# Optimization experiments

Hardware: AMD Instinct MI355X
Metric: run time of the kernel (lower is better)

Reference implementation:

```python
import jax, jax.numpy as jnp
import numpy as np

DEPTH, DIM, HEADS, MLP_HID, POS_DIM, PROJ_DIM, NCLS, INP = 5, 128, 8, 256, 128, 128, 1000, 35
EPS = 1e-5

def _ln(x, g, b):
    m = x.mean(-1, keepdims=True)
    v = ((x - m) ** 2).mean(-1, keepdims=True)
    return (x - m) / jnp.sqrt(v + EPS) * g + b

def _gelu(x):
    return jax.nn.gelu(x, approximate=False)  # torch nn.GELU default (erf)

def setup_inputs() -> dict:
    key = jax.random.key(0)
    ks = iter(jax.random.split(key, 80))
    nxt = lambda: next(ks)
    B, N = 8, 1024
    w = lambda *s: (jax.random.normal(nxt(), s, jnp.float32) / np.sqrt(s[-2]).astype(np.float32))
    z = lambda *s: jnp.zeros(s, jnp.float32)
    o = lambda *s: jnp.ones(s, jnp.float32)
    node_feat = jax.random.normal(nxt(), (B, N, 3), jnp.float32)
    a = (jax.random.uniform(nxt(), (B, N, N)) < 0.01).astype(jnp.float32)
    adj = jnp.maximum(a, a.transpose(0, 2, 1))  # symmetric 0/1 adjacency
    lapl = jax.random.normal(nxt(), (B, N, 32), jnp.float32) * 0.1
    d = dict(
        node_feat=node_feat, adj=adj, lapl=lapl,
        cls_token=jax.random.normal(nxt(), (1, 1, DIM), jnp.float32),
        pe_w1=w(INP, 2 * INP), pe_b1=z(2 * INP),
        pe_w2=w(2 * INP, 2 * INP), pe_b2=z(2 * INP),
        pe_w3=w(2 * INP, 2 * INP), pe_b3=z(2 * INP),
        pe_lng=o(2 * INP), pe_lnb=z(2 * INP),
        pe_w4=w(2 * INP, POS_DIM), pe_b4=z(POS_DIM),
        blk_ln1_g=o(DEPTH, DIM), blk_ln1_b=z(DEPTH, DIM),
        blk_qkv_w=w(DEPTH, DIM, 3 * HEADS * DIM),
        blk_proj_w=w(DEPTH, HEADS * DIM, DIM), blk_proj_b=z(DEPTH, DIM),
        blk_gamma_w=jax.random.uniform(nxt(), (DEPTH, DIM, 2), jnp.float32) * 0.01,
        blk_gamma_b=z(DEPTH, 2),
        blk_ln2_g=o(DEPTH, DIM), blk_ln2_b=z(DEPTH, DIM),
        blk_mlp_w1=w(DEPTH, DIM, MLP_HID), blk_mlp_b1=z(DEPTH, MLP_HID),
        blk_mlp_w2=w(DEPTH, MLP_HID, DIM), blk_mlp_b2=z(DEPTH, DIM),
        head_lng=o(DIM), head_lnb=z(DIM), head_w=w(DIM, DIM), head_b=z(DIM),
        proj_w1=w(DIM, PROJ_DIM), proj_b1=z(PROJ_DIM),
        proj_w2=w(PROJ_DIM, PROJ_DIM), proj_b2=z(PROJ_DIM),
        proj_w3=w(PROJ_DIM, PROJ_DIM), proj_b3=z(PROJ_DIM),
        proj_lng=o(PROJ_DIM), proj_lnb=z(PROJ_DIM),
        proj_w4=w(PROJ_DIM, NCLS), proj_b4=z(NCLS),
    )
    return d

def reference(node_feat, adj, lapl, cls_token, pe_w1, pe_b1, pe_w2, pe_b2, pe_w3, pe_b3,
              pe_lng, pe_lnb, pe_w4, pe_b4, blk_ln1_g, blk_ln1_b, blk_qkv_w, blk_proj_w,
              blk_proj_b, blk_gamma_w, blk_gamma_b, blk_ln2_g, blk_ln2_b, blk_mlp_w1,
              blk_mlp_b1, blk_mlp_w2, blk_mlp_b2, head_lng, head_lnb, head_w, head_b,
              proj_w1, proj_b1, proj_w2, proj_b2, proj_w3, proj_b3, proj_lng, proj_lnb,
              proj_w4, proj_b4):
    B, N, _ = node_feat.shape
    M = N + 1
    # positional-encoding MLP on concatenated [node_feat | lapl] (inp_dim = 35)
    x = jnp.concatenate([node_feat, lapl], axis=2)
    x = _gelu(x @ pe_w1 + pe_b1)
    x = _gelu(x @ pe_w2 + pe_b2)
    x = _gelu(x @ pe_w3 + pe_b3)
    x = _ln(x, pe_lng, pe_lnb) @ pe_w4 + pe_b4  # [B,N,DIM]
    x = jnp.concatenate([jnp.broadcast_to(cls_token, (B, 1, DIM)), x], axis=1)  # [B,M,DIM]
    # adjacency with cls row/col, adj_cls[:,0,0] = 1
    adj_cls = jnp.zeros((B, M, M), x.dtype).at[:, 0, 0].set(1.0).at[:, 1:, 1:].set(adj)
    scale = DIM ** (-0.5)
    for i in range(DEPTH):
        h = _ln(x, blk_ln1_g[i], blk_ln1_b[i])
        qkv = (h @ blk_qkv_w[i]).reshape(B, M, 3, HEADS, DIM).transpose(2, 0, 3, 1, 4)
        q, k, v = qkv[0], qkv[1], qkv[2]  # each [B,H,M,D]
        attn = jnp.einsum('bhnd,bhmd->bhnm', q, k) * scale
        gamma = jnp.exp(h @ blk_gamma_w[i] + blk_gamma_b[i])  # [B,M,2], use_exp=True
        attn = gamma[:, None, :, 0:1] * attn + gamma[:, None, :, 1:2] * adj_cls[:, None]
        attn = jax.nn.softmax(attn, axis=-1)
        o = jnp.einsum('bhnm,bhmd->bhnd', attn, v).transpose(0, 2, 1, 3).reshape(B, M, HEADS * DIM)
        x = o @ blk_proj_w[i] + blk_proj_b[i] + h  # residual from normed input (as in source)
        h2 = _ln(x, blk_ln2_g[i], blk_ln2_b[i])
        x = _gelu(h2 @ blk_mlp_w1[i] + blk_mlp_b1[i]) @ blk_mlp_w2[i] + blk_mlp_b2[i] + h2
    c = x[:, 0]
    c = _ln(c, head_lng, head_lnb) @ head_w + head_b  # mlp_head
    p = _gelu(c @ proj_w1 + proj_b1)
    p = _gelu(p @ proj_w2 + proj_b2)
    p = _gelu(p @ proj_w3 + proj_b3)
    p = _ln(p, proj_lng, proj_lnb) @ proj_w4 + proj_b4
    return (c, p)
```

## Files before the change

### kernel.cpp

```cpp
#include <hip/hip_runtime.h>
#include <hip/hip_bf16.h>
#include <math.h>

#define NB 8
#define NSEQ 1024
#define M_ 1025
#define ROWS (NB * M_)
#define DIMC 128
#define NHEADS 8
#define QKV3 3072
#define PEROWS (NB * NSEQ)
#define ACS 1088

typedef __attribute__((ext_vector_type(8))) short bf16x8;
typedef __attribute__((ext_vector_type(4))) float f32x4;

__device__ __forceinline__ float gelu_f(float x) {
  return 0.5f * x * (1.f + erff(x * 0.70710678118654752440f));
}

__device__ __forceinline__ unsigned short f2bf(float f) {
  __hip_bfloat16 h = __float2bfloat16(f);
  return *reinterpret_cast<unsigned short*>(&h);
}

__device__ __forceinline__ float bf2f(unsigned short u) {
  union { unsigned int i; float f; } c;
  c.i = ((unsigned int)u) << 16;
  return c.f;
}

template<int TR>
__global__ __launch_bounds__(256) void rowgemm_k(
    const float* __restrict__ in, const float* __restrict__ W,
    const float* __restrict__ bias, const float* __restrict__ res,
    float* __restrict__ out, int rows, int K, int Nout, int act, int remap)
{
  extern __shared__ float s_in[];
  const int tid = threadIdx.x;
  const int r0 = blockIdx.x * TR;
  const int tot = TR * K;
  for (int idx = tid; idx < tot; idx += blockDim.x) {
    int r = idx / K;
    int k = idx - r * K;
    int gr = r0 + r;
    s_in[idx] = (gr < rows) ? in[(size_t)gr * K + k] : 0.f;
  }
  __syncthreads();
  const int j = blockIdx.y * blockDim.x + tid;
  if (j >= Nout) return;
  float acc[TR];
  const float bv = bias ? bias[j] : 0.f;
#pragma unroll
  for (int r = 0; r < TR; ++r) acc[r] = bv;
  for (int k = 0; k < K; ++k) {
    const float w = W[(size_t)k * Nout + j];
#pragma unroll
    for (int r = 0; r < TR; ++r) acc[r] = fmaf(s_in[r * K + k], w, acc[r]);
  }
  for (int r = 0; r < TR; ++r) {
    const int gr = r0 + r;
    if (gr >= rows) break;
    float v = acc[r];
    if (act == 1) v = gelu_f(v);
    if (res) v += res[(size_t)gr * Nout + j];
    const size_t orow = remap ? (size_t)(gr + gr / 1024 + 1) : (size_t)gr;
    out[orow * (size_t)Nout + j] = v;
  }
}

template<int ACT, int OBF, int RES>
__global__ __launch_bounds__(256) void mgemm_k(
    const unsigned short* __restrict__ Xb, const unsigned short* __restrict__ Wt,
    const float* __restrict__ bias, const float* __restrict__ res,
    void* __restrict__ outp, int rows, int K, int N)
{
  __shared__ unsigned short sX[64][72];
  __shared__ unsigned short sW[64][72];
  const int tid = threadIdx.x;
  const int w = tid >> 6, lane = tid & 63;
  const int col = lane & 15, quad = lane >> 4;
  const int r0 = blockIdx.x * 64, n0 = blockIdx.y * 64;
  const int lr = tid >> 2, lc = tid & 3;
  const int xrow = min(r0 + lr, rows - 1);
  const unsigned short* xsrc = Xb + (size_t)xrow * K + lc * 8;
  const unsigned short* wsrc = Wt + (size_t)(n0 + lr) * K + lc * 8;

  f32x4 acc[4];
#pragma unroll
  for (int t = 0; t < 4; ++t) acc[t] = (f32x4){0.f, 0.f, 0.f, 0.f};

  for (int k0 = 0; k0 < K; k0 += 64) {
    __syncthreads();
    *(uint4*)&sX[lr][lc * 8]      = *(const uint4*)(xsrc + k0);
    *(uint4*)&sX[lr][lc * 8 + 32] = *(const uint4*)(xsrc + k0 + 32);
    *(uint4*)&sW[lr][lc * 8]      = *(const uint4*)(wsrc + k0);
    *(uint4*)&sW[lr][lc * 8 + 32] = *(const uint4*)(wsrc + k0 + 32);
    __syncthreads();
    const bf16x8 aX0 = *(const bf16x8*)&sX[w * 16 + col][quad * 8];
    const bf16x8 aX1 = *(const bf16x8*)&sX[w * 16 + col][32 + quad * 8];
#pragma unroll
    for (int t = 0; t < 4; ++t) {
      const bf16x8 bW0 = *(const bf16x8*)&sW[t * 16 + col][quad * 8];
      const bf16x8 bW1 = *(const bf16x8*)&sW[t * 16 + col][32 + quad * 8];
      acc[t] = __builtin_amdgcn_mfma_f32_16x16x32_bf16(aX0, bW0, acc[t], 0, 0, 0);
      acc[t] = __builtin_amdgcn_mfma_f32_16x16x32_bf16(aX1, bW1, acc[t], 0, 0, 0);
    }
  }
  const int gr_base = r0 + w * 16 + quad * 4;
#pragma unroll
  for (int t = 0; t < 4; ++t) {
    const int n = n0 + t * 16 + col;
    const float bv = bias ? bias[n] : 0.f;
#pragma unroll
    for (int r = 0; r < 4; ++r) {
      const int gr = gr_base + r;
      if (gr < rows) {
        float v = acc[t][r] + bv;
        if (ACT) v = gelu_f(v);
        if (RES) v += res[(size_t)gr * N + n];
        if (OBF) ((unsigned short*)outp)[(size_t)gr * N + n] = f2bf(v);
        else     ((float*)outp)[(size_t)gr * N + n] = v;
      }
    }
  }
}

template<int OBF>
__global__ __launch_bounds__(256) void mgemm128_k(
    const unsigned short* __restrict__ Xb, const unsigned short* __restrict__ Wt,
    const float* __restrict__ bias, void* __restrict__ outp,
    int rows, int K, int N)
{
  __shared__ unsigned short sX[128][72];
  __shared__ unsigned short sW[128][72];
  const int tid = threadIdx.x;
  const int w = tid >> 6, lane = tid & 63;
  const int col = lane & 15, quad = lane >> 4;
  const int wr = w >> 1, wc = w & 1;
  const int r0 = blockIdx.x * 128, n0 = blockIdx.y * 128;

  f32x4 acc[4][4];
#pragma unroll
  for (int i = 0; i < 4; ++i)
#pragma unroll
    for (int j = 0; j < 4; ++j) acc[i][j] = (f32x4){0.f, 0.f, 0.f, 0.f};

  for (int k0 = 0; k0 < K; k0 += 64) {
    __syncthreads();
#pragma unroll
    for (int l = 0; l < 4; ++l) {
      const int idx = l * 256 + tid;
      const int row = idx >> 3, c = idx & 7;
      const int xrow = min(r0 + row, rows - 1);
      *(uint4*)&sX[row][c * 8] = *(const uint4*)(Xb + (size_t)xrow * K + k0 + c * 8);
      *(uint4*)&sW[row][c * 8] = *(const uint4*)(Wt + (size_t)(n0 + row) * K + k0 + c * 8);
    }
    __syncthreads();
    bf16x8 aX[4][2];
#pragma unroll
    for (int i = 0; i < 4; ++i) {
      aX[i][0] = *(const bf16x8*)&sX[wr * 64 + i * 16 + col][quad * 8];
      aX[i][1] = *(const bf16x8*)&sX[wr * 64 + i * 16 + col][32 + quad * 8];
    }
#pragma unroll
    for (int j = 0; j < 4; ++j) {
      const bf16x8 b0 = *(const bf16x8*)&sW[wc * 64 + j * 16 + col][quad * 8];
      const bf16x8 b1 = *(const bf16x8*)&sW[wc * 64 + j * 16 + col][32 + quad * 8];
#pragma unroll
      for (int i = 0; i < 4; ++i) {
        acc[i][j] = __builtin_amdgcn_mfma_f32_16x16x32_bf16(aX[i][0], b0, acc[i][j], 0, 0, 0);
        acc[i][j] = __builtin_amdgcn_mfma_f32_16x16x32_bf16(aX[i][1], b1, acc[i][j], 0, 0, 0);
      }
    }
  }
#pragma unroll
  for (int i = 0; i < 4; ++i) {
    const int gr_base = r0 + wr * 64 + i * 16 + quad * 4;
#pragma unroll
    for (int j = 0; j < 4; ++j) {
      const int n = n0 + wc * 64 + j * 16 + col;
      const float bv = bias ? bias[n] : 0.f;
#pragma unroll
      for (int r = 0; r < 4; ++r) {
        const int gr = gr_base + r;
        if (gr < rows) {
          const float v = acc[i][j][r] + bv;
          if (OBF) ((unsigned short*)outp)[(size_t)gr * N + n] = f2bf(v);
          else     ((float*)outp)[(size_t)gr * N + n] = v;
        }
      }
    }
  }
}

__global__ __launch_bounds__(256) void ln_rows_k(
    const float* __restrict__ in, float* __restrict__ out,
    unsigned short* __restrict__ outb,
    const float* __restrict__ g, const float* __restrict__ b,
    const float* __restrict__ gw, const float* __restrict__ gb,
    float* __restrict__ gamout, int rows, int D)
{
  const int wv = (blockIdx.x * blockDim.x + threadIdx.x) >> 6;
  const int lane = threadIdx.x & 63;
  if (wv >= rows) return;
  const float* r = in + (size_t)wv * D;
  float s = 0.f;
  for (int d = lane; d < D; d += 64) s += r[d];
  for (int off = 32; off; off >>= 1) s += __shfl_down(s, off);
  const float mean = __shfl(s, 0) / (float)D;
  float v = 0.f;
  for (int d = lane; d < D; d += 64) { float t = r[d] - mean; v += t * t; }
  for (int off = 32; off; off >>= 1) v += __shfl_down(v, off);
  const float inv = rsqrtf(__shfl(v, 0) / (float)D + 1e-5f);
  float* orow = out + (size_t)wv * D;
  float a0 = 0.f, a1 = 0.f;
  for (int d = lane; d < D; d += 64) {
    const float o = (r[d] - mean) * inv * g[d] + b[d];
    orow[d] = o;
    if (outb) outb[(size_t)wv * D + d] = f2bf(o);
    if (gw) { a0 = fmaf(o, gw[2 * d], a0); a1 = fmaf(o, gw[2 * d + 1], a1); }
  }
  if (gw) {
    for (int off = 32; off; off >>= 1) { a0 += __shfl_down(a0, off); a1 += __shfl_down(a1, off); }
    if (lane == 0) {
      gamout[(size_t)wv * 2 + 0] = expf(a0 + gb[0]);
      gamout[(size_t)wv * 2 + 1] = expf(a1 + gb[1]);
    }
  }
}

__global__ void adjc_k(const float* __restrict__ adj, unsigned short* __restrict__ adjc)
{
  const int n = blockIdx.x;
  const int b = blockIdx.y;
  unsigned short* row = adjc + ((size_t)b * M_ + n) * ACS;
  const float* ar = (n >= 1) ? adj + ((size_t)b * NSEQ + (n - 1)) * NSEQ : nullptr;
  for (int m = threadIdx.x; m < ACS; m += 256) {
    float v = 0.f;
    if (n == 0) v = (m == 0) ? 1.f : 0.f;
    else if (m >= 1 && m <= NSEQ) v = ar[m - 1];
    row[m] = f2bf(v);
  }
}

__global__ void wtrans_k(const float* __restrict__ W, unsigned short* __restrict__ Wt,
                         int K, int N)
{
  __shared__ float t[32][33];
  const int k0 = blockIdx.x * 32, n0 = blockIdx.y * 32;
  const float* Wd = W + (size_t)blockIdx.z * K * N;
  unsigned short* Wtd = Wt + (size_t)blockIdx.z * K * N;
  for (int i = threadIdx.y; i < 32; i += 8)
    t[i][threadIdx.x] = Wd[(size_t)(k0 + i) * N + n0 + threadIdx.x];
  __syncthreads();
  for (int i = threadIdx.y; i < 32; i += 8)
    Wtd[(size_t)(n0 + i) * K + k0 + threadIdx.x] = f2bf(t[threadIdx.x][i]);
}

__global__ __launch_bounds__(256) void vtrans_k(
    const unsigned short* __restrict__ qkv, unsigned short* __restrict__ vt)
{
  __shared__ unsigned short sT[64][136];
  const int mt = blockIdx.x, hh = blockIdx.y, b = blockIdx.z;
  const int tid = threadIdx.x;
  const int m0 = mt * 64;
#pragma unroll
  for (int l = 0; l < 4; ++l) {
    const int idx = l * 256 + tid;
    const int m = idx >> 4, c = idx & 15;
    const int gm = m0 + m;
    uint4 v = make_uint4(0u, 0u, 0u, 0u);
    if (gm < M_) v = *(const uint4*)(qkv + ((size_t)(b * M_ + gm)) * QKV3 + 2048 + hh * DIMC + c * 8);
    *(uint4*)&sT[m][c * 8] = v;
  }
  __syncthreads();
#pragma unroll
  for (int l = 0; l < 4; ++l) {
    const int idx = l * 256 + tid;
    const int d = idx >> 3, mc = idx & 7;
    unsigned short tmp[8];
#pragma unroll
    for (int j = 0; j < 8; ++j) tmp[j] = sT[mc * 8 + j][d];
    *(uint4*)(vt + (((size_t)(b * NHEADS + hh) * DIMC + d) * ACS) + m0 + mc * 8) = *(uint4*)tmp;
  }
}

__global__ __launch_bounds__(256) void attn_mfma_k(
    const unsigned short* __restrict__ qkv, const float* __restrict__ gamma,
    const unsigned short* __restrict__ adjc, const unsigned short* __restrict__ vt,
    unsigned short* __restrict__ o)
{
  __shared__ unsigned short sK[64][136];
  __shared__ unsigned short sVt[128][72];
  __shared__ unsigned short sP[64][72];

  const int hh = blockIdx.x, qt = blockIdx.y, b = blockIdx.z;
  const int tid = threadIdx.x;
  const int w = tid >> 6;
  const int lane = tid & 63;
  const int col = lane & 15;
  const int quad = lane >> 4;
  const int n0 = qt * 64;
  const int qbase = n0 + w * 16;
  const float scale = 0.088388347648318447f;

  bf16x8 aQ[4];
  {
    const int qrow = min(qbase + col, 1024);
    const unsigned short* qp = qkv + ((size_t)(b * M_ + qrow)) * QKV3 + hh * DIMC + quad * 8;
#pragma unroll
    for (int c = 0; c < 4; ++c) aQ[c] = *(const bf16x8*)(qp + c * 32);
  }
  float g0[4], g1[4];
  const unsigned short* adjr[4];
#pragma unroll
  for (int r = 0; r < 4; ++r) {
    const int nc = min(qbase + quad * 4 + r, 1024);
    g0[r] = gamma[(size_t)(b * M_ + nc) * 2 + 0] * scale;
    g1[r] = gamma[(size_t)(b * M_ + nc) * 2 + 1];
    adjr[r] = adjc + ((size_t)b * M_ + nc) * ACS;
  }

  float l_i[4] = {0.f, 0.f, 0.f, 0.f};
  f32x4 Oacc[8];
#pragma unroll
  for (int t = 0; t < 8; ++t) Oacc[t] = (f32x4){0.f, 0.f, 0.f, 0.f};

  const size_t vtbase = ((size_t)(b * NHEADS + hh)) * DIMC * ACS;

  for (int kt = 0; kt < 17; ++kt) {
    const int m0 = kt * 64;
    __syncthreads();
#pragma unroll
    for (int l = 0; l < 4; ++l) {
      const int idx = l * 256 + tid;
      {
        const int m = idx >> 4, c = idx & 15;
        const int gm = m0 + m;
        uint4 kv = make_uint4(0u, 0u, 0u, 0u);
        if (gm < M_) kv = *(const uint4*)(qkv + ((size_t)(b * M_ + gm)) * QKV3 + 1024 + hh * DIMC + c * 8);
        *(uint4*)&sK[m][c * 8] = kv;
      }
      {
        const int d = idx >> 3, mc = idx & 7;
        const uint4 vv = *(const uint4*)(vt + vtbase + (size_t)d * ACS + m0 + mc * 8);
        const int swc = mc ^ ((d >> 3) & 7);
        *(uint4*)&sVt[d][swc * 8] = vv;
      }
    }
    __syncthreads();

    f32x4 Sacc[4];
#pragma unroll
    for (int t = 0; t < 4; ++t) Sacc[t] = (f32x4){0.f, 0.f, 0.f, 0.f};
#pragma unroll
    for (int t = 0; t < 4; ++t) {
#pragma unroll
      for (int c = 0; c < 4; ++c) {
        const bf16x8 bK = *(const bf16x8*)&sK[t * 16 + col][c * 32 + quad * 8];
        Sacc[t] = __builtin_amdgcn_mfma_f32_16x16x32_bf16(aQ[c], bK, Sacc[t], 0, 0, 0);
      }
    }

#pragma unroll
    for (int t = 0; t < 4; ++t) {
      const int m = m0 + t * 16 + col;
      const bool mv = (m < M_);
      const int chb = t * 2 + (col >> 3);
#pragma unroll
      for (int r = 0; r < 4; ++r) {
        const float av = bf2f(adjr[r][m]);
        const float s = fmaf(g0[r], Sacc[t][r], g1[r] * av);
        const float pv = mv ? __expf(s) : 0.f;
        l_i[r] += pv;
        const int ql = w * 16 + quad * 4 + r;
        sP[ql][((chb ^ (ql & 7)) * 8) + (col & 7)] = f2bf(pv);
      }
    }

#pragma unroll
    for (int ch = 0; ch < 2; ++ch) {
      const int r0a = w * 16 + col;
      const bf16x8 aP = *(const bf16x8*)&sP[r0a][(((ch * 4 + quad) ^ (col & 7)) * 8)];
#pragma unroll
      for (int t = 0; t < 8; ++t) {
        const int pc = (ch * 4 + quad) ^ ((t * 2 + (col >> 3)) & 7);
        const bf16x8 bV = *(const bf16x8*)&sVt[t * 16 + col][pc * 8];
        Oacc[t] = __builtin_amdgcn_mfma_f32_16x16x32_bf16(aP, bV, Oacc[t], 0, 0, 0);
      }
    }
  }

#pragma unroll
  for (int r = 0; r < 4; ++r) {
    float s = l_i[r];
    s += __shfl_xor(s, 1);
    s += __shfl_xor(s, 2);
    s += __shfl_xor(s, 4);
    s += __shfl_xor(s, 8);
    const int n = qbase + quad * 4 + r;
    if (n < M_) {
      const float invl = 1.f / s;
      unsigned short* orow = o + ((size_t)(b * M_ + n)) * (NHEADS * DIMC) + hh * DIMC + col;
#pragma unroll
      for (int t = 0; t < 8; ++t) orow[t * 16] = f2bf(Oacc[t][r] * invl);
    }
  }
}

__global__ void concat_pe_k(const float* __restrict__ nf, const float* __restrict__ lp,
                            float* __restrict__ x35, int rows)
{
  const int idx = blockIdx.x * blockDim.x + threadIdx.x;
  if (idx >= rows * 35) return;
  const int r = idx / 35, c = idx - r * 35;
  x35[idx] = (c < 3) ? nf[(size_t)r * 3 + c] : lp[(size_t)r * 32 + (c - 3)];
}

__global__ void fill_cls_k(const float* __restrict__ cls, float* __restrict__ x)
{
  x[(size_t)blockIdx.x * M_ * DIMC + threadIdx.x] = cls[threadIdx.x];
}

__global__ void extract_cls_k(const float* __restrict__ x, float* __restrict__ c0)
{
  c0[(size_t)blockIdx.x * DIMC + threadIdx.x] = x[(size_t)blockIdx.x * M_ * DIMC + threadIdx.x];
}

extern "C" void kernel_launch(void* const* d_in, const int* in_sizes, int n_in,
                              void* d_out, int out_size, void* d_ws, size_t ws_size,
                              hipStream_t stream)
{
  (void)in_sizes; (void)n_in; (void)out_size; (void)ws_size;
  const float* node_feat = (const float*)d_in[0];
  const float* adj       = (const float*)d_in[1];
  const float* lapl      = (const float*)d_in[2];
  const float* cls_token = (const float*)d_in[3];
  const float* pe_w1 = (const float*)d_in[4];
  const float* pe_b1 = (const float*)d_in[5];
  const float* pe_w2 = (const float*)d_in[6];
  const float* pe_b2 = (const float*)d_in[7];
  const float* pe_w3 = (const float*)d_in[8];
  const float* pe_b3 = (const float*)d_in[9];
  const float* pe_lng = (const float*)d_in[10];
  const float* pe_lnb = (const float*)d_in[11];
  const float* pe_w4 = (const float*)d_in[12];
  const float* pe_b4 = (const float*)d_in[13];
  const float* blk_ln1_g = (const float*)d_in[14];
  const float* blk_ln1_b = (const float*)d_in[15];
  const float* blk_qkv_w = (const float*)d_in[16];
  const float* blk_proj_w = (const float*)d_in[17];
  const float* blk_proj_b = (const float*)d_in[18];
  const float* blk_gamma_w = (const float*)d_in[19];
  const float* blk_gamma_b = (const float*)d_in[20];
  const float* blk_ln2_g = (const float*)d_in[21];
  const float* blk_ln2_b = (const float*)d_in[22];
  const float* blk_mlp_w1 = (const float*)d_in[23];
  const float* blk_mlp_b1 = (const float*)d_in[24];
  const float* blk_mlp_w2 = (const float*)d_in[25];
  const float* blk_mlp_b2 = (const float*)d_in[26];
  const float* head_lng = (const float*)d_in[27];
  const float* head_lnb = (const float*)d_in[28];
  const float* head_w = (const float*)d_in[29];
  const float* head_b = (const float*)d_in[30];
  const float* proj_w1 = (const float*)d_in[31];
  const float* proj_b1 = (const float*)d_in[32];
  const float* proj_w2 = (const float*)d_in[33];
  const float* proj_b2 = (const float*)d_in[34];
  const float* proj_w3 = (const float*)d_in[35];
  const float* proj_b3 = (const float*)d_in[36];
  const float* proj_lng = (const float*)d_in[37];
  const float* proj_lnb = (const float*)d_in[38];
  const float* proj_w4 = (const float*)d_in[39];
  const float* proj_b4 = (const float*)d_in[40];

  float* ws   = (float*)d_ws;
  float* x    = ws;
  float* h    = x + 1049600;
  float* gam  = h + 1049600;
  float* obuf = gam + 16400;
  unsigned short* obufb = (unsigned short*)obuf;
  unsigned short* hidb  = (unsigned short*)(obuf + 4198400);
  float* x35 = obuf;
  float* xa  = obuf + 300000;
  float* xb  = obuf + 900000;
  float* sm  = obuf + 5248000;
  unsigned short* hb   = (unsigned short*)(sm + 8192);
  unsigned short* qkv  = hb + 1049600;
  unsigned short* adjc = qkv + 25190400;
  unsigned short* vt   = adjc + 8921600;
  unsigned short* qkvWt = vt + 8912896;
  unsigned short* projWt = qkvWt + 5 * 393216;
  unsigned short* mlp1Wt = projWt + 5 * 131072;
  unsigned short* mlp2Wt = mlp1Wt + 5 * 32768;
  float* s0 = sm, *s1 = sm + 1024, *s2 = sm + 2048, *s3 = sm + 3072;

  float* out_c = (float*)d_out;
  float* out_p = out_c + NB * DIMC;

  adjc_k<<<dim3(M_, NB), 256, 0, stream>>>(adj, adjc);
  wtrans_k<<<dim3(4, 96, 5), dim3(32, 8), 0, stream>>>(blk_qkv_w, qkvWt, 128, 3072);
  wtrans_k<<<dim3(32, 4, 5), dim3(32, 8), 0, stream>>>(blk_proj_w, projWt, 1024, 128);
  wtrans_k<<<dim3(4, 8, 5), dim3(32, 8), 0, stream>>>(blk_mlp_w1, mlp1Wt, 128, 256);
  wtrans_k<<<dim3(8, 4, 5), dim3(32, 8), 0, stream>>>(blk_mlp_w2, mlp2Wt, 256, 128);

  concat_pe_k<<<(PEROWS * 35 + 255) / 256, 256, 0, stream>>>(node_feat, lapl, x35, PEROWS);
  rowgemm_k<16><<<dim3(512, 1), 128, 16 * 35 * 4, stream>>>(x35, pe_w1, pe_b1, nullptr, xa, PEROWS, 35, 70, 1, 0);
  rowgemm_k<16><<<dim3(512, 1), 128, 16 * 70 * 4, stream>>>(xa, pe_w2, pe_b2, nullptr, xb, PEROWS, 70, 70, 1, 0);
  rowgemm_k<16><<<dim3(512, 1), 128, 16 * 70 * 4, stream>>>(xb, pe_w3, pe_b3, nullptr, xa, PEROWS, 70, 70, 1, 0);
  ln_rows_k<<<(PEROWS * 64 + 255) / 256, 256, 0, stream>>>(xa, xb, nullptr, pe_lng, pe_lnb, nullptr, nullptr, nullptr, PEROWS, 70);
  rowgemm_k<16><<<dim3(512, 1), 128, 16 * 70 * 4, stream>>>(xb, pe_w4, pe_b4, nullptr, x, PEROWS, 70, DIMC, 0, 1);
  fill_cls_k<<<NB, DIMC, 0, stream>>>(cls_token, x);

  const int lnGrid = (ROWS * 64 + 255) / 256;
  for (int i = 0; i < 5; ++i) {
    const float* ln1g = blk_ln1_g + i * DIMC;
    const float* ln1b = blk_ln1_b + i * DIMC;
    const float* pb   = blk_proj_b + i * DIMC;
    const float* gw   = blk_gamma_w + (size_t)i * DIMC * 2;
    const float* gb   = blk_gamma_b + i * 2;
    const float* ln2g = blk_ln2_g + i * DIMC;
    const float* ln2b = blk_ln2_b + i * DIMC;
    const float* mb1  = blk_mlp_b1 + i * 256;
    const float* mb2  = blk_mlp_b2 + i * DIMC;
    const unsigned short* qw = qkvWt + (size_t)i * 393216;
    const unsigned short* pw = projWt + (size_t)i * 131072;
    const unsigned short* m1w = mlp1Wt + (size_t)i * 32768;
    const unsigned short* m2w = mlp2Wt + (size_t)i * 32768;

    ln_rows_k<<<lnGrid, 256, 0, stream>>>(x, h, hb, ln1g, ln1b, gw, gb, gam, ROWS, DIMC);
    mgemm128_k<1><<<dim3(65, 24), 256, 0, stream>>>(hb, qw, nullptr, qkv, ROWS, 128, 3072);
    vtrans_k<<<dim3(17, NHEADS, NB), 256, 0, stream>>>(qkv, vt);
    attn_mfma_k<<<dim3(NHEADS, 17, NB), 256, 0, stream>>>(qkv, gam, adjc, vt, obufb);
    mgemm_k<0, 0, 1><<<dim3(129, 2), 256, 0, stream>>>(obufb, pw, pb, h, x, ROWS, 1024, 128);
    ln_rows_k<<<lnGrid, 256, 0, stream>>>(x, h, hb, ln2g, ln2b, nullptr, nullptr, nullptr, ROWS, DIMC);
    mgemm_k<1, 1, 0><<<dim3(129, 4), 256, 0, stream>>>(hb, m1w, mb1, nullptr, hidb, ROWS, 128, 256);
    mgemm_k<0, 0, 1><<<dim3(129, 2), 256, 0, stream>>>(hidb, m2w, mb2, h, x, ROWS, 256, 128);
  }

  extract_cls_k<<<NB, DIMC, 0, stream>>>(x, s0);
  ln_rows_k<<<2, 256, 0, stream>>>(s0, s1, nullptr, head_lng, head_lnb, nullptr, nullptr, nullptr, NB, DIMC);
  rowgemm_k<8><<<dim3(1, 1), 128, 8 * 128 * 4, stream>>>(s1, head_w, head_b, nullptr, out_c, NB, DIMC, DIMC, 0, 0);
  rowgemm_k<8><<<dim3(1, 1), 128, 8 * 128 * 4, stream>>>(out_c, proj_w1, proj_b1, nullptr, s2, NB, DIMC, DIMC, 1, 0);
  rowgemm_k<8><<<dim3(1, 1), 128, 8 * 128 * 4, stream>>>(s2, proj_w2, proj_b2, nullptr, s3, NB, DIMC, DIMC, 1, 0);
  rowgemm_k<8><<<dim3(1, 1), 128, 8 * 128 * 4, stream>>>(s3, proj_w3, proj_b3, nullptr, s2, NB, DIMC, DIMC, 1, 0);
  ln_rows_k<<<2, 256, 0, stream>>>(s2, s3, nullptr, proj_lng, proj_lnb, nullptr, nullptr, nullptr, NB, DIMC);
  rowgemm_k<8><<<dim3(1, 4), 256, 8 * 128 * 4, stream>>>(s3, proj_w4, proj_b4, nullptr, out_p, NB, DIMC, 1000, 0, 0);
}
```

Measured before the change: 1.622 ms.

## Bit-pack adjacency mask and run attention as a two-tile-per-block grid

Replaces the dense bf16 adjacency matrix with a 64-bit ballot bitmask per row and 64-column chunk. The attention kernel loads one mask word per row per key tile instead of gathering bf16 values from global memory, which cuts adjacency traffic roughly sixteenfold. The attention grid is also flattened to 544 blocks, each processing two (head, query-tile, batch) tiles in sequence. This reduces block count and may affect load balance and occupancy.

New measurement: 1.821 ms. 1.12x slower.

```diff
diff --git a/kernel.cpp b/kernel.cpp
--- a/kernel.cpp
+++ b/kernel.cpp
@@ -230,17 +230,19 @@
   }
 }
 
-__global__ void adjc_k(const float* __restrict__ adj, unsigned short* __restrict__ adjc)
+__global__ __launch_bounds__(256) void adjp_k(const float* __restrict__ adj,
+                                              unsigned long long* __restrict__ adjp)
 {
   const int n = blockIdx.x;
   const int b = blockIdx.y;
-  unsigned short* row = adjc + ((size_t)b * M_ + n) * ACS;
-  const float* ar = (n >= 1) ? adj + ((size_t)b * NSEQ + (n - 1)) * NSEQ : nullptr;
-  for (int m = threadIdx.x; m < ACS; m += 256) {
-    float v = 0.f;
-    if (n == 0) v = (m == 0) ? 1.f : 0.f;
-    else if (m >= 1 && m <= NSEQ) v = ar[m - 1];
-    row[m] = f2bf(v);
+  const int wv = threadIdx.x >> 6, lane = threadIdx.x & 63;
+  for (int w = wv; w < 17; w += 4) {
+    const int m = w * 64 + lane;
+    float av = 0.f;
+    if (n == 0) av = (m == 0) ? 1.f : 0.f;
+    else if (m >= 1 && m <= NSEQ) av = adj[((size_t)b * NSEQ + (n - 1)) * NSEQ + (m - 1)];
+    const unsigned long long mask = __ballot(av != 0.f);
+    if (lane == 0) adjp[((size_t)b * M_ + n) * 17 + w] = mask;
   }
 }
 
@@ -288,123 +290,135 @@
 
 __global__ __launch_bounds__(256) void attn_mfma_k(
     const unsigned short* __restrict__ qkv, const float* __restrict__ gamma,
-    const unsigned short* __restrict__ adjc, const unsigned short* __restrict__ vt,
+    const unsigned long long* __restrict__ adjp, const unsigned short* __restrict__ vt,
     unsigned short* __restrict__ o)
 {
   __shared__ unsigned short sK[64][136];
   __shared__ unsigned short sVt[128][72];
   __shared__ unsigned short sP[64][72];
 
-  const int hh = blockIdx.x, qt = blockIdx.y, b = blockIdx.z;
   const int tid = threadIdx.x;
   const int w = tid >> 6;
   const int lane = tid & 63;
   const int col = lane & 15;
   const int quad = lane >> 4;
-  const int n0 = qt * 64;
-  const int qbase = n0 + w * 16;
   const float scale = 0.088388347648318447f;
 
-  bf16x8 aQ[4];
-  {
-    const int qrow = min(qbase + col, 1024);
-    const unsigned short* qp = qkv + ((size_t)(b * M_ + qrow)) * QKV3 + hh * DIMC + quad * 8;
-#pragma unroll
-    for (int c = 0; c < 4; ++c) aQ[c] = *(const bf16x8*)(qp + c * 32);
-  }
-  float g0[4], g1[4];
-  const unsigned short* adjr[4];
-#pragma unroll
-  for (int r = 0; r < 4; ++r) {
-    const int nc = min(qbase + quad * 4 + r, 1024);
-    g0[r] = gamma[(size_t)(b * M_ + nc) * 2 + 0] * scale;
-    g1[r] = gamma[(size_t)(b * M_ + nc) * 2 + 1];
-    adjr[r] = adjc + ((size_t)b * M_ + nc) * ACS;
-  }
-
-  float l_i[4] = {0.f, 0.f, 0.f, 0.f};
-  f32x4 Oacc[8];
-#pragma unroll
-  for (int t = 0; t < 8; ++t) Oacc[t] = (f32x4){0.f, 0.f, 0.f, 0.f};
-
-  const size_t vtbase = ((size_t)(b * NHEADS + hh)) * DIMC * ACS;
-
-  for (int kt = 0; kt < 17; ++kt) {
-    const int m0 = kt * 64;
-    __syncthreads();
-#pragma unroll
-    for (int l = 0; l < 4; ++l) {
-      const int idx = l * 256 + tid;
-      {
-        const int m = idx >> 4, c = idx & 15;
-        const int gm = m0 + m;
-        uint4 kv = make_uint4(0u, 0u, 0u, 0u);
-        if (gm < M_) kv = *(const uint4*)(qkv + ((size_t)(b * M_ + gm)) * QKV3 + 1024 + hh * DIMC + c * 8);
-        *(uint4*)&sK[m][c * 8] = kv;
-      }
-      {
-        const int d = idx >> 3, mc = idx & 7;
-        const uint4 vv = *(const uint4*)(vt + vtbase + (size_t)d * ACS + m0 + mc * 8);
-        const int swc = mc ^ ((d >> 3) & 7);
-        *(uint4*)&sVt[d][swc * 8] = vv;
-      }
-    }
-    __syncthreads();
-
-    f32x4 Sacc[4];
-#pragma unroll
-    for (int t = 0; t < 4; ++t) Sacc[t] = (f32x4){0.f, 0.f, 0.f, 0.f};
-#pragma unroll
-    for (int t = 0; t < 4; ++t) {
-#pragma unroll
-      for (int c = 0; c < 4; ++c) {
-        const bf16x8 bK = *(const bf16x8*)&sK[t * 16 + col][c * 32 + quad * 8];
-        Sacc[t] = __builtin_amdgcn_mfma_f32_16x16x32_bf16(aQ[c], bK, Sacc[t], 0, 0, 0);
-      }
-    }
-
-#pragma unroll
-    for (int t = 0; t < 4; ++t) {
-      const int m = m0 + t * 16 + col;
-      const bool mv = (m < M_);
-      const int chb = t * 2 + (col >> 3);
-#pragma unroll
-      for (int r = 0; r < 4; ++r) {
-        const float av = bf2f(adjr[r][m]);
-        const float s = fmaf(g0[r], Sacc[t][r], g1[r] * av);
-        const float pv = mv ? __expf(s) : 0.f;
-        l_i[r] += pv;
-        const int ql = w * 16 + quad * 4 + r;
-        sP[ql][((chb ^ (ql & 7)) * 8) + (col & 7)] = f2bf(pv);
-      }
-    }
-
-#pragma unroll
-    for (int ch = 0; ch < 2; ++ch) {
-      const int r0a = w * 16 + col;
-      const bf16x8 aP = *(const bf16x8*)&sP[r0a][(((ch * 4 + quad) ^ (col & 7)) * 8)];
-#pragma unroll
-      for (int t = 0; t < 8; ++t) {
-        const int pc = (ch * 4 + quad) ^ ((t * 2 + (col >> 3)) & 7);
-        const bf16x8 bV = *(const bf16x8*)&sVt[t * 16 + col][pc * 8];
-        Oacc[t] = __builtin_amdgcn_mfma_f32_16x16x32_bf16(aP, bV, Oacc[t], 0, 0, 0);
-      }
-    }
-  }
-
-#pragma unroll
-  for (int r = 0; r < 4; ++r) {
-    float s = l_i[r];
-    s += __shfl_xor(s, 1);
-    s += __shfl_xor(s, 2);
-    s += __shfl_xor(s, 4);
-    s += __shfl_xor(s, 8);
-    const int n = qbase + quad * 4 + r;
-    if (n < M_) {
-      const float invl = 1.f / s;
-      unsigned short* orow = o + ((size_t)(b * M_ + n)) * (NHEADS * DIMC) + hh * DIMC + col;
-#pragma unroll
-      for (int t = 0; t < 8; ++t) orow[t * 16] = f2bf(Oacc[t][r] * invl);
+  for (int it = 0; it < 2; ++it) {
+    const int tile = blockIdx.x + it * 544;
+    const int hh = tile & 7;
+    const int rest = tile >> 3;
+    const int qt = rest % 17;
+    const int b = rest / 17;
+    const int n0 = qt * 64;
+    const int qbase = n0 + w * 16;
+
+    bf16x8 aQ[4];
+    {
+      const int qrow = min(qbase + col, 1024);
+      const unsigned short* qp = qkv + ((size_t)(b * M_ + qrow)) * QKV3 + hh * DIMC + quad * 8;
+#pragma unroll
+      for (int c = 0; c < 4; ++c) aQ[c] = *(const bf16x8*)(qp + c * 32);
+    }
+    float g0[4], g1[4];
+    size_t adjo[4];
+#pragma unroll
+    for (int r = 0; r < 4; ++r) {
+      const int nc = min(qbase + quad * 4 + r, 1024);
+      g0[r] = gamma[(size_t)(b * M_ + nc) * 2 + 0] * scale;
+      g1[r] = gamma[(size_t)(b * M_ + nc) * 2 + 1];
+      adjo[r] = ((size_t)b * M_ + nc) * 17;
+    }
+
+    float l_i[4] = {0.f, 0.f, 0.f, 0.f};
+    f32x4 Oacc[8];
+#pragma unroll
+    for (int t = 0; t < 8; ++t) Oacc[t] = (f32x4){0.f, 0.f, 0.f, 0.f};
+
+    const size_t vtbase = ((size_t)(b * NHEADS + hh)) * DIMC * ACS;
+
+    for (int kt = 0; kt < 17; ++kt) {
+      const int m0 = kt * 64;
+      __syncthreads();
+#pragma unroll
+      for (int l = 0; l < 4; ++l) {
+        const int idx = l * 256 + tid;
+        {
+          const int m = idx >> 4, c = idx & 15;
+          const int gm = m0 + m;
+          uint4 kv = make_uint4(0u, 0u, 0u, 0u);
+          if (gm < M_) kv = *(const uint4*)(qkv + ((size_t)(b * M_ + gm)) * QKV3 + 1024 + hh * DIMC + c * 8);
+          *(uint4*)&sK[m][c * 8] = kv;
+        }
+        {
+          const int d = idx >> 3, mc = idx & 7;
+          const uint4 vv = *(const uint4*)(vt + vtbase + (size_t)d * ACS + m0 + mc * 8);
+          const int swc = mc ^ ((d >> 3) & 7);
+          *(uint4*)&sVt[d][swc * 8] = vv;
+        }
+      }
+      __syncthreads();
+
+      unsigned long long mk[4];
+#pragma unroll
+      for (int r = 0; r < 4; ++r) mk[r] = adjp[adjo[r] + kt];
+
+      f32x4 Sacc[4];
+#pragma unroll
+      for (int t = 0; t < 4; ++t) Sacc[t] = (f32x4){0.f, 0.f, 0.f, 0.f};
+#pragma unroll
+      for (int t = 0; t < 4; ++t) {
+#pragma unroll
+        for (int c = 0; c < 4; ++c) {
+          const bf16x8 bK = *(const bf16x8*)&sK[t * 16 + col][c * 32 + quad * 8];
+          Sacc[t] = __builtin_amdgcn_mfma_f32_16x16x32_bf16(aQ[c], bK, Sacc[t], 0, 0, 0);
+        }
+      }
+
+#pragma unroll
+      for (int t = 0; t < 4; ++t) {
+        const int m = m0 + t * 16 + col;
+        const bool mv = (m < M_);
+        const int chb = t * 2 + (col >> 3);
+        const int sh = t * 16 + col;
+#pragma unroll
+        for (int r = 0; r < 4; ++r) {
+          const float bias = ((mk[r] >> sh) & 1ull) ? g1[r] : 0.f;
+          const float s = fmaf(g0[r], Sacc[t][r], bias);
+          const float pv = mv ? __expf(s) : 0.f;
+          l_i[r] += pv;
+          const int ql = w * 16 + quad * 4 + r;
+          sP[ql][((chb ^ (ql & 7)) * 8) + (col & 7)] = f2bf(pv);
+        }
+      }
+
+#pragma unroll
+      for (int ch = 0; ch < 2; ++ch) {
+        const int r0a = w * 16 + col;
+        const bf16x8 aP = *(const bf16x8*)&sP[r0a][(((ch * 4 + quad) ^ (col & 7)) * 8)];
+#pragma unroll
+        for (int t = 0; t < 8; ++t) {
+          const int pc = (ch * 4 + quad) ^ ((t * 2 + (col >> 3)) & 7);
+          const bf16x8 bV = *(const bf16x8*)&sVt[t * 16 + col][pc * 8];
+          Oacc[t] = __builtin_amdgcn_mfma_f32_16x16x32_bf16(aP, bV, Oacc[t], 0, 0, 0);
+        }
+      }
+    }
+
+#pragma unroll
+    for (int r = 0; r < 4; ++r) {
+      float s = l_i[r];
+      s += __shfl_xor(s, 1);
+      s += __shfl_xor(s, 2);
+      s += __shfl_xor(s, 4);
+      s += __shfl_xor(s, 8);
+      const int n = qbase + quad * 4 + r;
+      if (n < M_) {
+        const float invl = 1.f / s;
+        unsigned short* orow = o + ((size_t)(b * M_ + n)) * (NHEADS * DIMC) + hh * DIMC + col;
+#pragma unroll
+        for (int t = 0; t < 8; ++t) orow[t * 16] = f2bf(Oacc[t][r] * invl);
+      }
     }
   }
 }
@@ -488,8 +502,8 @@
   float* sm  = obuf + 5248000;
   unsigned short* hb   = (unsigned short*)(sm + 8192);
   unsigned short* qkv  = hb + 1049600;
-  unsigned short* adjc = qkv + 25190400;
-  unsigned short* vt   = adjc + 8921600;
+  unsigned long long* adjp = (unsigned long long*)(qkv + 25190400);
+  unsigned short* vt   = (unsigned short*)(adjp + 139400 + 88);
   unsigned short* qkvWt = vt + 8912896;
   unsigned short* projWt = qkvWt + 5 * 393216;
   unsigned short* mlp1Wt = projWt + 5 * 131072;
@@ -499,7 +513,7 @@
   float* out_c = (float*)d_out;
   float* out_p = out_c + NB * DIMC;
 
-  adjc_k<<<dim3(M_, NB), 256, 0, stream>>>(adj, adjc);
+  adjp_k<<<dim3(M_, NB), 256, 0, stream>>>(adj, adjp);
   wtrans_k<<<dim3(4, 96, 5), dim3(32, 8), 0, stream>>>(blk_qkv_w, qkvWt, 128, 3072);
   wtrans_k<<<dim3(32, 4, 5), dim3(32, 8), 0, stream>>>(blk_proj_w, projWt, 1024, 128);
   wtrans_k<<<dim3(4, 8, 5), dim3(32, 8), 0, stream>>>(blk_mlp_w1, mlp1Wt, 128, 256);
@@ -532,7 +546,7 @@
     ln_rows_k<<<lnGrid, 256, 0, stream>>>(x, h, hb, ln1g, ln1b, gw, gb, gam, ROWS, DIMC);
     mgemm128_k<1><<<dim3(65, 24), 256, 0, stream>>>(hb, qw, nullptr, qkv, ROWS, 128, 3072);
     vtrans_k<<<dim3(17, NHEADS, NB), 256, 0, stream>>>(qkv, vt);
-    attn_mfma_k<<<dim3(NHEADS, 17, NB), 256, 0, stream>>>(qkv, gam, adjc, vt, obufb);
+    attn_mfma_k<<<dim3(544), 256, 0, stream>>>(qkv, gam, adjp, vt, obufb);
     mgemm_k<0, 0, 1><<<dim3(129, 2), 256, 0, stream>>>(obufb, pw, pb, h, x, ROWS, 1024, 128);
     ln_rows_k<<<lnGrid, 256, 0, stream>>>(x, h, hb, ln2g, ln2b, nullptr, nullptr, nullptr, ROWS, DIMC);
     mgemm_k<1, 1, 0><<<dim3(129, 4), 256, 0, stream>>>(hb, m1w, mb1, nullptr, hidb, ROWS, 128, 256);
```
